# Performance work log

Measured on AMD Instinct MI355X. Metric: run time of the kernel, lower is better.

Reference implementation:

```python
import jax, jax.numpy as jnp
import numpy as np

B, IN, H = 128, 512, 1024

def setup_inputs() -> dict:
    key = jax.random.key(0)
    ks = jax.random.split(key, 20)
    def lin(kw, kb, out_dim, in_dim):
        lim = 1.0 / np.sqrt(in_dim)
        W = jax.random.uniform(kw, (out_dim, in_dim), minval=-lim, maxval=lim)
        b = jax.random.uniform(kb, (out_dim,), minval=-lim, maxval=lim)
        return W, b
    W1, b1 = lin(ks[0], ks[1], H, IN)
    W2, b2 = lin(ks[2], ks[3], H, H)
    W3, b3 = lin(ks[4], ks[5], H, H)
    Wc, bc = lin(ks[6], ks[7], 1, H)
    Wr, br = lin(ks[8], ks[9], H, 1)
    Wn, bn = lin(ks[10], ks[11], 2, H)
    Wv, bv = lin(ks[12], ks[13], 1, H)
    alpha = 0.01 * (2.0 * jax.random.uniform(ks[14], (H, H)) - 1.0)
    items = jax.random.normal(ks[15], (B, IN))
    plastic_weights = jax.random.normal(ks[16], (B, H, H))
    reward = jax.random.normal(ks[17], (B, 1))
    return dict(items=items, plastic_weights=plastic_weights, reward=reward,
                W1=W1, b1=b1, W2=W2, b2=b2, W3=W3, b3=b3,
                Wc=Wc, bc=bc, Wr=Wr, br=br, Wn=Wn, bn=bn,
                alpha=alpha, Wv=Wv, bv=bv)

def reference(items, plastic_weights, reward, W1, b1, W2, b2, W3, b3,
              Wc, bc, Wr, br, Wn, bn, alpha, Wv, bv):
    # nonlinear item embeddings: [B, H]
    emb = jnp.tanh(items @ W1.T + b1)
    current = emb @ W2.T + b2  # [B, H]
    # elementwise-scaled batched GEMV: (alpha * plastic)[b,h,i] @ emb[b,i]
    plastic_contrib = jnp.einsum('bhi,bi->bh', alpha * plastic_weights, emb)
    pre_tanh_hidden = current + plastic_contrib
    hidden = jnp.tanh(pre_tanh_hidden)
    reward_emb = reward @ Wr.T + br  # [B, H]
    nm_out = jnp.tanh((jnp.tanh((hidden + reward_emb) @ W3.T + b3)) @ Wn.T + bn)  # [B, 2]
    neuromodulator = (nm_out[:, 0] - nm_out[:, 1])[:, None, None]  # [B,1,1]
    choice = jax.nn.sigmoid(hidden @ Wc.T + bc)  # [B, 1]
    value = hidden @ Wv.T + bv  # [B, 1]
    # Hebbian outer-product trace: [B, H, H]
    hebbian = jnp.tanh(jnp.einsum('bh,bi->bhi', pre_tanh_hidden, emb)) * 10.0
    new_plastic = jnp.clip(plastic_weights + neuromodulator * hebbian, -50.0, 50.0)
    return (choice, neuromodulator, value, new_plastic, hidden)
```

## Files before the change

kernel.cpp:

```cpp
#include <hip/hip_runtime.h>
#include <hip/hip_bf16.h>

#define BATCH 128
#define IN_DIM 512
#define HDIM 1024

typedef __attribute__((ext_vector_type(4))) float f32x4;

__device__ __forceinline__ float fast_tanh(float x) {
    float e = __expf(2.0f * x);
    return 1.0f - 2.0f * __builtin_amdgcn_rcpf(e + 1.0f);
}

__global__ __launch_bounds__(256) void k1_emb(
    const float* __restrict__ items, const float* __restrict__ W1,
    const float* __restrict__ b1, float* __restrict__ emb_f)
{
    __shared__ float it[IN_DIM];
    int b = blockIdx.x, t = threadIdx.x;
    it[t] = items[b * IN_DIM + t];
    it[t + 256] = items[b * IN_DIM + t + 256];
    __syncthreads();
    #pragma unroll
    for (int j = 0; j < 4; ++j) {
        int h = t + 256 * j;
        const float* wrow = W1 + h * IN_DIM;
        float acc = 0.f;
        #pragma unroll 4
        for (int c = 0; c < IN_DIM; c += 4) {
            f32x4 w = *reinterpret_cast<const f32x4*>(wrow + c);
            acc += w[0] * it[c] + w[1] * it[c + 1] + w[2] * it[c + 2] + w[3] * it[c + 3];
        }
        emb_f[b * HDIM + h] = tanhf(acc + b1[h]);
    }
}

__global__ __launch_bounds__(256) void k2_hidden(
    const float* __restrict__ plastic, const float* __restrict__ alpha,
    const float* __restrict__ W2, const float* __restrict__ b2,
    const float* __restrict__ emb_f, float* __restrict__ pre_f, float* __restrict__ hid_f)
{
    int bid = blockIdx.x;
    int b = bid >> 8;
    int h = ((bid & 255) << 2) + (threadIdx.x >> 6);
    int l = threadIdx.x & 63;
    const float* prow = plastic + (((size_t)b) << 20) + ((size_t)h << 10);
    const float* arow = alpha + (h << 10);
    const float* wrow = W2 + (h << 10);
    const float* erow = emb_f + (b << 10);
    float acc = 0.f;
    #pragma unroll
    for (int c = 0; c < 4; ++c) {
        int i = c * 256 + l * 4;
        f32x4 p = *reinterpret_cast<const f32x4*>(prow + i);
        f32x4 a = *reinterpret_cast<const f32x4*>(arow + i);
        f32x4 w = *reinterpret_cast<const f32x4*>(wrow + i);
        f32x4 e = *reinterpret_cast<const f32x4*>(erow + i);
        acc += e[0] * fmaf(a[0], p[0], w[0]);
        acc += e[1] * fmaf(a[1], p[1], w[1]);
        acc += e[2] * fmaf(a[2], p[2], w[2]);
        acc += e[3] * fmaf(a[3], p[3], w[3]);
    }
    #pragma unroll
    for (int off = 32; off > 0; off >>= 1) acc += __shfl_xor(acc, off);
    if (l == 0) {
        float pre = acc + b2[h];
        pre_f[(b << 10) + h] = pre;
        hid_f[(b << 10) + h] = tanhf(pre);
    }
}

__global__ __launch_bounds__(256) void k3a_t3(
    const float* __restrict__ hid_f, const float* __restrict__ reward,
    const float* __restrict__ Wr, const float* __restrict__ br,
    const float* __restrict__ W3, const float* __restrict__ b3,
    float* __restrict__ t3_f)
{
    int bid = blockIdx.x;
    int b = bid >> 8;
    int h = ((bid & 255) << 2) + (threadIdx.x >> 6);
    int l = threadIdx.x & 63;
    float rw = reward[b];
    const float* wrow = W3 + (h << 10);
    const float* hrow = hid_f + (b << 10);
    float acc = 0.f;
    #pragma unroll
    for (int c = 0; c < 4; ++c) {
        int i = c * 256 + l * 4;
        f32x4 w  = *reinterpret_cast<const f32x4*>(wrow + i);
        f32x4 wr = *reinterpret_cast<const f32x4*>(Wr + i);
        f32x4 bb = *reinterpret_cast<const f32x4*>(br + i);
        f32x4 hh = *reinterpret_cast<const f32x4*>(hrow + i);
        #pragma unroll
        for (int j = 0; j < 4; ++j)
            acc += (hh[j] + fmaf(rw, wr[j], bb[j])) * w[j];
    }
    #pragma unroll
    for (int off = 32; off > 0; off >>= 1) acc += __shfl_xor(acc, off);
    if (l == 0) t3_f[(b << 10) + h] = tanhf(acc + b3[h]);
}

__global__ __launch_bounds__(256) void k3b_heads(
    const float* __restrict__ t3_f, const float* __restrict__ hid_f,
    const float* __restrict__ Wn, const float* __restrict__ bn,
    const float* __restrict__ Wc, const float* __restrict__ bc,
    const float* __restrict__ Wv, const float* __restrict__ bv,
    float* __restrict__ nm_f, float* __restrict__ out)
{
    int b = blockIdx.x, t = threadIdx.x;
    int w = t >> 6, l = t & 63;
    const float* src = (w < 2) ? (t3_f + (b << 10)) : (hid_f + (b << 10));
    const float* wv = (w == 0) ? Wn : (w == 1) ? (Wn + HDIM) : (w == 2) ? Wc : Wv;
    float acc = 0.f;
    #pragma unroll
    for (int c = 0; c < 4; ++c) {
        int i = c * 256 + l * 4;
        f32x4 wg = *reinterpret_cast<const f32x4*>(wv + i);
        f32x4 ss = *reinterpret_cast<const f32x4*>(src + i);
        acc += ss[0] * wg[0] + ss[1] * wg[1] + ss[2] * wg[2] + ss[3] * wg[3];
    }
    #pragma unroll
    for (int off = 32; off > 0; off >>= 1) acc += __shfl_xor(acc, off);
    __shared__ float red[4];
    if (l == 0) red[w] = acc;
    __syncthreads();
    if (t == 0) {
        float nm0 = tanhf(red[0] + bn[0]);
        float nm1 = tanhf(red[1] + bn[1]);
        float nm = nm0 - nm1;
        nm_f[b] = nm;
        out[BATCH + b] = nm;
        out[b] = 1.0f / (1.0f + __expf(-(red[2] + bc[0])));
        out[2 * BATCH + b] = red[3] + bv[0];
    }
    const size_t HID_OFF = (size_t)3 * BATCH + (size_t)BATCH * HDIM * HDIM;
    for (int i = t; i < HDIM; i += 256)
        out[HID_OFF + (size_t)b * HDIM + i] = hid_f[(b << 10) + i];
}

__global__ __launch_bounds__(256) void k4_update(
    const float* __restrict__ plastic, const float* __restrict__ emb_f,
    const float* __restrict__ pre_f, const float* __restrict__ nm_f,
    float* __restrict__ outp)
{
    size_t idx = ((size_t)blockIdx.x * 256 + threadIdx.x) * 4;
    int b   = (int)(idx >> 20);
    int rem = (int)(idx & 1048575u);
    int h   = rem >> 10;
    int i0  = rem & 1023;
    float nm  = nm_f[b];
    float pre = pre_f[(b << 10) + h];
    f32x4 p = *reinterpret_cast<const f32x4*>(plastic + idx);
    f32x4 e = *reinterpret_cast<const f32x4*>(emb_f + (b << 10) + i0);
    f32x4 o;
    #pragma unroll
    for (int j = 0; j < 4; ++j) {
        float heb = fast_tanh(pre * e[j]) * 10.0f;
        float v = fmaf(nm, heb, p[j]);
        o[j] = fminf(fmaxf(v, -50.0f), 50.0f);
    }
    *reinterpret_cast<f32x4*>(outp + idx) = o;
}

extern "C" void kernel_launch(void* const* d_in, const int* in_sizes, int n_in,
                              void* d_out, int out_size, void* d_ws, size_t ws_size,
                              hipStream_t stream)
{
    const float* items   = (const float*)d_in[0];
    const float* plastic = (const float*)d_in[1];
    const float* reward  = (const float*)d_in[2];
    const float* W1 = (const float*)d_in[3];
    const float* b1 = (const float*)d_in[4];
    const float* W2 = (const float*)d_in[5];
    const float* b2 = (const float*)d_in[6];
    const float* W3 = (const float*)d_in[7];
    const float* b3 = (const float*)d_in[8];
    const float* Wc = (const float*)d_in[9];
    const float* bc = (const float*)d_in[10];
    const float* Wr = (const float*)d_in[11];
    const float* br = (const float*)d_in[12];
    const float* Wn = (const float*)d_in[13];
    const float* bn = (const float*)d_in[14];
    const float* alpha = (const float*)d_in[15];
    const float* Wv = (const float*)d_in[16];
    const float* bv = (const float*)d_in[17];

    float* ws    = (float*)d_ws;
    float* emb_f = ws;
    float* pre_f = ws + 131072;
    float* hid_f = ws + 262144;
    float* t3_f  = ws + 393216;
    float* nm_f  = ws + 524288;

    float* out  = (float*)d_out;
    float* outp = out + 384;

    k1_emb   <<<BATCH, 256, 0, stream>>>(items, W1, b1, emb_f);
    k2_hidden<<<(BATCH * HDIM) / 4, 256, 0, stream>>>(plastic, alpha, W2, b2, emb_f, pre_f, hid_f);
    k3a_t3   <<<(BATCH * HDIM) / 4, 256, 0, stream>>>(hid_f, reward, Wr, br, W3, b3, t3_f);
    k3b_heads<<<BATCH, 256, 0, stream>>>(t3_f, hid_f, Wn, bn, Wc, bc, Wv, bv, nm_f, out);
    k4_update<<<(size_t)(BATCH * HDIM) * HDIM / 1024, 256, 0, stream>>>(plastic, emb_f, pre_f, nm_f, outp);
}
```

Measured before the change: 456.9 us.

## Reuse alpha/W2 rows across batch chunk, reverse update order, nontemporal stores

k2_hidden now keeps each thread's alpha and W2 slices in registers and loops over a chunk of 8 batches, so those weights are no longer reloaded once per batch. k4_update walks the plastic tensor in reverse, so the most recently read parts of plastic (the tail, read last by k2) are processed first while they may still sit in the last-level cache. Its output writes use nontemporal stores to avoid polluting the cache. The trade-offs are fewer blocks and more registers in k2, and a cache-reuse bet that depends on cache size versus the 512MB plastic tensor.

```diff
diff --git a/kernel.cpp b/kernel.cpp
--- a/kernel.cpp
+++ b/kernel.cpp
@@ -4,6 +4,7 @@
 #define BATCH 128
 #define IN_DIM 512
 #define HDIM 1024
+#define BCHUNK 8
 
 typedef __attribute__((ext_vector_type(4))) float f32x4;
 
@@ -40,33 +41,46 @@
     const float* __restrict__ W2, const float* __restrict__ b2,
     const float* __restrict__ emb_f, float* __restrict__ pre_f, float* __restrict__ hid_f)
 {
-    int bid = blockIdx.x;
-    int b = bid >> 8;
-    int h = ((bid & 255) << 2) + (threadIdx.x >> 6);
-    int l = threadIdx.x & 63;
-    const float* prow = plastic + (((size_t)b) << 20) + ((size_t)h << 10);
+    int hg = blockIdx.x & 255;
+    int bc = blockIdx.x >> 8;
+    int w  = threadIdx.x >> 6;
+    int l  = threadIdx.x & 63;
+    int h  = (hg << 2) + w;
+
     const float* arow = alpha + (h << 10);
     const float* wrow = W2 + (h << 10);
-    const float* erow = emb_f + (b << 10);
-    float acc = 0.f;
+    f32x4 ar[4], wr[4];
     #pragma unroll
     for (int c = 0; c < 4; ++c) {
         int i = c * 256 + l * 4;
-        f32x4 p = *reinterpret_cast<const f32x4*>(prow + i);
-        f32x4 a = *reinterpret_cast<const f32x4*>(arow + i);
-        f32x4 w = *reinterpret_cast<const f32x4*>(wrow + i);
-        f32x4 e = *reinterpret_cast<const f32x4*>(erow + i);
-        acc += e[0] * fmaf(a[0], p[0], w[0]);
-        acc += e[1] * fmaf(a[1], p[1], w[1]);
-        acc += e[2] * fmaf(a[2], p[2], w[2]);
-        acc += e[3] * fmaf(a[3], p[3], w[3]);
-    }
-    #pragma unroll
-    for (int off = 32; off > 0; off >>= 1) acc += __shfl_xor(acc, off);
-    if (l == 0) {
-        float pre = acc + b2[h];
-        pre_f[(b << 10) + h] = pre;
-        hid_f[(b << 10) + h] = tanhf(pre);
+        ar[c] = *reinterpret_cast<const f32x4*>(arow + i);
+        wr[c] = *reinterpret_cast<const f32x4*>(wrow + i);
+    }
+    float b2h = b2[h];
+
+    #pragma unroll 2
+    for (int bb = 0; bb < BCHUNK; ++bb) {
+        int b = bc * BCHUNK + bb;
+        const float* prow = plastic + (((size_t)b) << 20) + ((size_t)h << 10);
+        const float* erow = emb_f + (b << 10);
+        float acc = 0.f;
+        #pragma unroll
+        for (int c = 0; c < 4; ++c) {
+            int i = c * 256 + l * 4;
+            f32x4 p = *reinterpret_cast<const f32x4*>(prow + i);
+            f32x4 e = *reinterpret_cast<const f32x4*>(erow + i);
+            acc += e[0] * fmaf(ar[c][0], p[0], wr[c][0]);
+            acc += e[1] * fmaf(ar[c][1], p[1], wr[c][1]);
+            acc += e[2] * fmaf(ar[c][2], p[2], wr[c][2]);
+            acc += e[3] * fmaf(ar[c][3], p[3], wr[c][3]);
+        }
+        #pragma unroll
+        for (int off = 32; off > 0; off >>= 1) acc += __shfl_xor(acc, off);
+        if (l == 0) {
+            float pre = acc + b2h;
+            pre_f[(b << 10) + h] = pre;
+            hid_f[(b << 10) + h] = tanhf(pre);
+        }
     }
 }
 
@@ -143,7 +157,9 @@
     const float* __restrict__ pre_f, const float* __restrict__ nm_f,
     float* __restrict__ outp)
 {
-    size_t idx = ((size_t)blockIdx.x * 256 + threadIdx.x) * 4;
+    const size_t NG = (size_t)BATCH * HDIM * HDIM / 4;
+    size_t gid = (size_t)blockIdx.x * 256 + threadIdx.x;
+    size_t idx = (NG - 1 - gid) * 4;
     int b   = (int)(idx >> 20);
     int rem = (int)(idx & 1048575u);
     int h   = rem >> 10;
@@ -159,7 +175,7 @@
         float v = fmaf(nm, heb, p[j]);
         o[j] = fminf(fmaxf(v, -50.0f), 50.0f);
     }
-    *reinterpret_cast<f32x4*>(outp + idx) = o;
+    __builtin_nontemporal_store(o, reinterpret_cast<f32x4*>(outp + idx));
 }
 
 extern "C" void kernel_launch(void* const* d_in, const int* in_sizes, int n_in,
@@ -196,7 +212,7 @@
     float* outp = out + 384;
 
     k1_emb   <<<BATCH, 256, 0, stream>>>(items, W1, b1, emb_f);
-    k2_hidden<<<(BATCH * HDIM) / 4, 256, 0, stream>>>(plastic, alpha, W2, b2, emb_f, pre_f, hid_f);
+    k2_hidden<<<(HDIM / 4) * (BATCH / BCHUNK), 256, 0, stream>>>(plastic, alpha, W2, b2, emb_f, pre_f, hid_f);
     k3a_t3   <<<(BATCH * HDIM) / 4, 256, 0, stream>>>(hid_f, reward, Wr, br, W3, b3, t3_f);
     k3b_heads<<<BATCH, 256, 0, stream>>>(t3_f, hid_f, Wn, bn, Wc, bc, Wv, bv, nm_f, out);
     k4_update<<<(size_t)(BATCH * HDIM) * HDIM / 1024, 256, 0, stream>>>(plastic, emb_f, pre_f, nm_f, outp);
```

After: 406.7 us. 11.0% less time.
